# Optimization experiments

Hardware: AMD Instinct MI355X
Metric: run time of the kernel (lower is better)

Reference implementation:

```python
import jax, jax.numpy as jnp
import numpy as np

K_TOP = 2
N_HEADS = 4

def _ln(x, g, b, eps=1e-5):
    mu = x.mean(-1, keepdims=True)
    var = ((x - mu) ** 2).mean(-1, keepdims=True)
    return (x - mu) * jax.lax.rsqrt(var + eps) * g + b

def setup_inputs() -> dict:
    key = jax.random.key(0)
    ks = jax.random.split(key, 12)
    B, Na, dz, da = 1024, 32, 96, 32
    D = dz + da
    E, F, Hh, nr = 8, 1024, 512, 4
    s = 0.02
    rn = lambda k, sh: jax.random.normal(k, sh, jnp.float32) * s
    return dict(
        z=jax.random.normal(ks[0], (B, Na, dz), jnp.float32),
        a=jax.random.normal(ks[1], (B, Na, da), jnp.float32),
        w_gate=rn(ks[2], (Na * D, E)),
        w_in=rn(ks[3], (E, 3 * D, D)), b_in=jnp.zeros((E, 3 * D), jnp.float32),
        w_out=rn(ks[4], (E, D, D)), b_out=jnp.zeros((E, D), jnp.float32),
        ln1_g=jnp.ones((E, D), jnp.float32), ln1_b=jnp.zeros((E, D), jnp.float32),
        w1=rn(ks[5], (E, F, D)), b1=jnp.zeros((E, F), jnp.float32),
        w2=rn(ks[6], (E, D, F)), b2=jnp.zeros((E, D), jnp.float32),
        ln2_g=jnp.ones((E, D), jnp.float32), ln2_b=jnp.zeros((E, D), jnp.float32),
        head_w1=rn(ks[7], (Hh, Na * D)), head_b1=jnp.zeros((Hh,), jnp.float32),
        head_w2=rn(ks[8], (nr, Hh)), head_b2=jnp.zeros((nr,), jnp.float32),
    )

def reference(z, a, w_gate, w_in, b_in, w_out, b_out, ln1_g, ln1_b, w1, b1, w2, b2, ln2_g, ln2_b, head_w1, head_b1, head_w2, head_b2):
    B, Na, _ = z.shape
    x = jnp.concatenate([z, a], axis=-1)          # [B, Na, D]
    D = x.shape[-1]
    E = w_gate.shape[1]
    hd = D // N_HEADS
    x_flat = x.reshape(B, -1)                     # [B, Na*D]

    # --- NoisyTopKRouter (eval: clean logits only) ---
    logits = x_flat @ w_gate                      # [B, E]
    top_vals, top_idx = jax.lax.top_k(logits, min(K_TOP + 1, E))
    tk_gates = jax.nn.softmax(top_vals[:, :K_TOP], axis=1)
    gates = jnp.zeros_like(logits).at[jnp.arange(B)[:, None], top_idx[:, :K_TOP]].set(tk_gates)
    load = (gates > 0).sum(0).astype(jnp.float32)
    importance = gates.sum(0)
    cv2 = lambda v: jnp.var(v, ddof=1) / (jnp.mean(v) ** 2 + 1e-10)
    loss_bal = cv2(importance) + cv2(load) + jax.scipy.special.logsumexp(logits, axis=-1).mean()

    # --- expert (self-attn + FFN, pre/post-LN residual) ---
    def expert(p):
        wi, bi, wo, bo, g1, be1, W1, B1, W2, B2, g2, be2 = p
        qkv = x @ wi.T + bi                       # [B, Na, 3D]
        q, k_, v = jnp.split(qkv, 3, axis=-1)
        q = q.reshape(B, Na, N_HEADS, hd)
        k_ = k_.reshape(B, Na, N_HEADS, hd)
        v = v.reshape(B, Na, N_HEADS, hd)
        sc = jnp.einsum('bqhd,bkhd->bhqk', q, k_) / jnp.sqrt(jnp.float32(hd))
        att = jax.nn.softmax(sc, axis=-1)
        o = jnp.einsum('bhqk,bkhd->bqhd', att, v).reshape(B, Na, D)
        o = o @ wo.T + bo
        h = _ln(x + o, g1, be1)
        f = jax.nn.relu(h @ W1.T + B1) @ W2.T + B2
        return _ln(h + f, g2, be2)

    def body(y, p):
        *ep, gate_e = p                           # gate_e: [B]
        y = y + gate_e[:, None, None] * expert(tuple(ep))
        return y, None

    xs = (w_in, b_in, w_out, b_out, ln1_g, ln1_b, w1, b1, w2, b2, ln2_g, ln2_b, gates.T)
    y, _ = jax.lax.scan(body, jnp.zeros_like(x), xs)

    y_flat = y.reshape(B, -1)
    r = jax.nn.relu(y_flat @ head_w1.T + head_b1) @ head_w2.T + head_b2  # [B, n_r]
    return r, gates, loss_bal
```

## Files before the change

kernel.cpp:

```cpp
#include <hip/hip_runtime.h>
#include <math.h>


typedef short bf16x8 __attribute__((ext_vector_type(8)));
typedef float f32x4 __attribute__((ext_vector_type(4)));
typedef unsigned short u16;

#define MFMA(a, b, c) __builtin_amdgcn_mfma_f32_16x16x32_bf16((a), (b), (c), 0, 0, 0)

__device__ __forceinline__ u16 f2bf(float f) {
    unsigned int u = __float_as_uint(f);
    unsigned int r = u + 0x7FFFu + ((u >> 16) & 1u);
    return (u16)(r >> 16);
}
__device__ __forceinline__ float bf2f(u16 s) {
    return __uint_as_float(((unsigned int)s) << 16);
}

__global__ __launch_bounds__(256) void convert_kernel(
    const float* __restrict__ wi, const float* __restrict__ wo,
    const float* __restrict__ w1, const float* __restrict__ w2,
    const float* __restrict__ hw1,
    u16* __restrict__ wiB, u16* __restrict__ woB, u16* __restrict__ w1B,
    u16* __restrict__ w2B, u16* __restrict__ hw1B)
// ... 49 lines not shown
        for (int e = 0; e < 8; ++e) L[e] = red[0][e];
        int i0 = 0;
#pragma unroll
        for (int e = 1; e < 8; ++e) if (L[e] > L[i0]) i0 = e;
        int i1 = -1; float v1 = -3.0e38f;
#pragma unroll
        for (int e = 0; e < 8; ++e) if (e != i0 && L[e] > v1) { v1 = L[e]; i1 = e; }
        float e1 = expf(v1 - L[i0]);
        float inv = 1.f / (1.f + e1);
        float g0 = inv, g1 = e1 * inv;
#pragma unroll
        for (int e = 0; e < 8; ++e)
            gates_out[b * 8 + e] = (e == i0) ? g0 : ((e == i1) ? g1 : 0.f);
        float m = L[i0];
        float se = 0.f;
#pragma unroll
        for (int e = 0; e < 8; ++e) se += expf(L[e] - m);
        lse_ws[b] = m + logf(se);
        topi[b * 2 + 0] = i0; topi[b * 2 + 1] = i1;
        topg[b * 2 + 0] = g0; topg[b * 2 + 1] = g1;
    }
}

__global__ __launch_bounds__(256) void loss_kernel(
    const float* __restrict__ gates, const float* __restrict__ lse,
    float* __restrict__ out_loss)
{
    __shared__ float red[17][256];
    const int t = threadIdx.x;
    float imp[8], ld[8]; float ls = 0.f;
#pragma unroll
    for (int e = 0; e < 8; ++e) { imp[e] = 0.f; ld[e] = 0.f; }
    for (int b = t; b < 1024; b += 256) {
#pragma unroll
        for (int e = 0; e < 8; ++e) {
            float g = gates[b * 8 + e];
            imp[e] += g;
            ld[e] += (g > 0.f) ? 1.f : 0.f;
        }
        ls += lse[b];
    }
#pragma unroll
    for (int e = 0; e < 8; ++e) { red[e][t] = imp[e]; red[8 + e][t] = ld[e]; }
    red[16][t] = ls;
    __syncthreads();
    for (int s = 128; s; s >>= 1) {
        if (t < s) {
            for (int q = 0; q < 17; ++q) red[q][t] += red[q][t + s];
        }
        __syncthreads();
    }
    if (t == 0) {
        float cv[2];
        for (int p = 0; p < 2; ++p) {
            float sum = 0.f;
            for (int e = 0; e < 8; ++e) sum += red[p * 8 + e][0];
            float mean = sum * (1.f / 8.f);
            float var = 0.f;
            for (int e = 0; e < 8; ++e) {
                float dd = red[p * 8 + e][0] - mean;
                var += dd * dd;
            }
            var *= (1.f / 7.f);
            cv[p] = var / (mean * mean + 1e-10f);
        }
        out_loss[0] = cv[0] + cv[1] + red[16][0] * (1.f / 1024.f);
    }
}

__global__ __launch_bounds__(1024) void build_kernel(
    const int* __restrict__ topi, int* __restrict__ cnts,
    int* __restrict__ ent, int* __restrict__ meta)
{
    __shared__ int sc_[8];
    __shared__ int toff[9];
    const int t = threadIdx.x;
    if (t < 8) sc_[t] = 0;
    __syncthreads();
    int e0 = topi[t * 2], e1 = topi[t * 2 + 1];
    int p0 = atomicAdd(&sc_[e0], 1);
    ent[e0 * 2048 + p0] = t * 2;
    int p1 = atomicAdd(&sc_[e1], 1);
    ent[e1 * 2048 + p1] = t * 2 + 1;
    __syncthreads();
    if (t == 0) {
        int off = 0;
        for (int e = 0; e < 8; ++e) { toff[e] = off; off += (sc_[e] + 3) >> 2; }
        toff[8] = off;
        meta[0] = off;
    }
    __syncthreads();
    if (t < 8) {
        cnts[t] = sc_[t];
        int ntl = (sc_[t] + 3) >> 2, o = toff[t];
        for (int j = 0; j < ntl; ++j) {
            meta[1 + 2 * (o + j)] = t;
            meta[2 + 2 * (o + j)] = j * 4;
        }
    }
}

#define SM_X  0
#define SM_Q  32768
#define SM_K  65536
#define SM_VT 98304
#define SM_P  131072
#define SM_PS 147456
#define SM_PQ 149504
#define SM_MU 151552
#define SM_RS 152064
#define SM_TOTAL 152576
#define NTILES 520

__global__ __launch_bounds__(512, 2) void expert_group_kernel(
    const float* __restrict__ z, const float* __restrict__ a,
    const u16* __restrict__ wiBF, const float* __restrict__ b_in,
    const u16* __restrict__ woBF, const float* __restrict__ b_out,
    const float* __restrict__ ln1g, const float* __restrict__ ln1b,
    const u16* __restrict__ w1BF, const float* __restrict__ b1,
    const u16* __restrict__ w2BF, const float* __restrict__ b2,
    const float* __restrict__ ln2g, const float* __restrict__ ln2b,
    const float* __restrict__ topg, const int* __restrict__ cnts,
    const int* __restrict__ meta, const int* __restrict__ ent,
    u16* __restrict__ ybf)
{
    __shared__ __align__(16) char sm[SM_TOTAL];
    const int n_tiles = meta[0];
    const int bid = blockIdx.x;
    if (bid >= n_tiles) return;
    const int e = meta[1 + 2 * bid], base = meta[2 + 2 * bid];
    const int cnt = cnts[e];

    const int t = threadIdx.x;
    const int w = t >> 6, l = t & 63, l16 = l & 15, lk = l >> 4;
    const int ke = lk * 8;
    const int wr = w >> 2, wc = w & 3;
    const f32x4 zv = {0.f, 0.f, 0.f, 0.f};

    int bs[4], valid[4]; float gg[4];
#pragma unroll
    for (int i = 0; i < 4; ++i) {
        int gi = base + i;
        int idx = (gi < cnt) ? gi : (cnt - 1);
        int code = ent[e * 2048 + idx];
        valid[i] = (gi < cnt);
        bs[i] = code;
        gg[i] = topg[code];
    }

    {
        const int grow = t >> 4;
        const int gcol = (t & 15) * 8;
#pragma unroll
        for (int i = 0; i < 4; ++i) {
            int b_ = bs[i] >> 1;
            float v[8];
            if (gcol < 96) {
                const float* zp = z + ((size_t)b_ * 32 + grow) * 96 + gcol;
                float4 p0 = *(const float4*)zp, p1 = *(const float4*)(zp + 4);
                v[0] = p0.x; v[1] = p0.y; v[2] = p0.z; v[3] = p0.w;
                v[4] = p1.x; v[5] = p1.y; v[6] = p1.z; v[7] = p1.w;
            } else {
                const float* ap = a + ((size_t)b_ * 32 + grow) * 32 + (gcol - 96);
                float4 p0 = *(const float4*)ap, p1 = *(const float4*)(ap + 4);
                v[0] = p0.x; v[1] = p0.y; v[2] = p0.z; v[3] = p0.w;
                v[4] = p1.x; v[5] = p1.y; v[6] = p1.z; v[7] = p1.w;
            }
            bf16x8 pk;
#pragma unroll
            for (int j = 0; j < 8; ++j) pk[j] = (short)f2bf(v[j]);
            int row = i * 32 + grow;
            *(bf16x8*)(sm + SM_X + row * 256 + ((gcol * 2) ^ ((row & 7) << 4))) = pk;
        }
    }
    __syncthreads();

    {
        f32x4 acc[4][6];
#pragma unroll
        for (int m = 0; m < 4; ++m)
#pragma unroll
            for (int q = 0; q < 6; ++q) acc[m][q] = zv;
#pragma unroll
        for (int ks = 0; ks < 4; ++ks) {
            int kb = (ks * 32 + ke) * 2;
            bf16x8 af[4];
#pragma unroll
            for (int m = 0; m < 4; ++m) {
                int R = wr * 64 + m * 16 + l16;
                af[m] = *(const bf16x8*)(sm + SM_X + R * 256 + (kb ^ ((R & 7) << 4)));
            }
#pragma unroll
            for (int q = 0; q < 6; ++q) {
                int j = wc * 96 + q * 16 + l16;
                bf16x8 bb = *(const bf16x8*)(wiBF + e * 49152 + j * 128 + ks * 32 + ke);
#pragma unroll
                for (int m = 0; m < 4; ++m) acc[m][q] = MFMA(af[m], bb, acc[m][q]);
            }
        }
#pragma unroll
        for (int q = 0; q < 6; ++q) {
            int C = wc * 96 + q * 16 + l16;
            float bj = b_in[e * 384 + C];
#pragma unroll
            for (int m = 0; m < 4; ++m)
#pragma unroll
                for (int i = 0; i < 4; ++i) {
                    int R = wr * 64 + m * 16 + lk * 4 + i;
                    u16 val = f2bf(acc[m][q][i] + bj);
                    if (C < 128) {
                        *(u16*)(sm + SM_Q + R * 256 + ((C * 2) ^ ((R & 7) << 4))) = val;
                    } else if (C < 256) {
                        int c2 = C - 128;
                        *(u16*)(sm + SM_K + R * 256 + ((c2 * 2) ^ ((R & 7) << 4))) = val;
                    } else {
                        int rv = C - 256;
                        *(u16*)(sm + SM_VT + rv * 256 + ((R * 2) ^ ((rv & 7) << 4))) = val;
                    }
                }
        }
    }
    __syncthreads();

    f32x4 Ofrag[2][2][2];
    {
        const int tok = w >> 1;
        const int h2 = (w & 1) * 2;
        const float scale = 0.17677669529663687f;
#pragma unroll
        for (int p = 0; p < 2; ++p) {
            const int hb = (h2 + p) * 32;
            bf16x8 qa[2], kb2[2];
#pragma unroll
            for (int mt = 0; mt < 2; ++mt) {
                int R = tok * 32 + mt * 16 + l16;
                qa[mt] = *(const bf16x8*)(sm + SM_Q + R * 256 + (((hb + ke) * 2) ^ ((R & 7) << 4)));
                kb2[mt] = *(const bf16x8*)(sm + SM_K + R * 256 + (((hb + ke) * 2) ^ ((R & 7) << 4)));
            }
            f32x4 sc[2][2];
            sc[0][0] = MFMA(qa[0], kb2[0], zv); sc[0][1] = MFMA(qa[0], kb2[1], zv);
            sc[1][0] = MFMA(qa[1], kb2[0], zv); sc[1][1] = MFMA(qa[1], kb2[1], zv);
#pragma unroll
            for (int mt = 0; mt < 2; ++mt)
#pragma unroll
                for (int i = 0; i < 4; ++i) {
                    float v0 = sc[mt][0][i] * scale, v1 = sc[mt][1][i] * scale;
                    float m = fmaxf(v0, v1);
                    m = fmaxf(m, __shfl_xor(m, 1)); m = fmaxf(m, __shfl_xor(m, 2));
                    m = fmaxf(m, __shfl_xor(m, 4)); m = fmaxf(m, __shfl_xor(m, 8));
                    float e0 = __expf(v0 - m), e1 = __expf(v1 - m);
                    float ssum = e0 + e1;
                    ssum += __shfl_xor(ssum, 1); ssum += __shfl_xor(ssum, 2);
                    ssum += __shfl_xor(ssum, 4); ssum += __shfl_xor(ssum, 8);
                    float inv = 1.f / ssum;
                    int row = mt * 16 + lk * 4 + i;
                    char* pb = sm + SM_P + w * 2048 + row * 64;
                    int sw = (row & 3) << 4;
                    *(u16*)(pb + ((l16 * 2) ^ sw)) = f2bf(e0 * inv);
                    *(u16*)(pb + (((16 + l16) * 2) ^ sw)) = f2bf(e1 * inv);
                }
            bf16x8 pa[2];
#pragma unroll
            for (int mt = 0; mt < 2; ++mt) {
                int row = mt * 16 + l16;
                pa[mt] = *(const bf16x8*)(sm + SM_P + w * 2048 + row * 64 +
                                          ((ke * 2) ^ ((row & 3) << 4)));
            }
#pragma unroll
            for (int nt = 0; nt < 2; ++nt) {
                int rv = hb + nt * 16 + l16;
                bf16x8 vb = *(const bf16x8*)(sm + SM_VT + rv * 256 +
                                             (((tok * 32 + ke) * 2) ^ ((rv & 7) << 4)));
                Ofrag[p][0][nt] = MFMA(pa[0], vb, zv);
                Ofrag[p][1][nt] = MFMA(pa[1], vb, zv);
            }
        }
#pragma unroll
        for (int p = 0; p < 2; ++p)
#pragma unroll
            for (int mt = 0; mt < 2; ++mt)
#pragma unroll
                for (int nt = 0; nt < 2; ++nt)
#pragma unroll
                    for (int i = 0; i < 4; ++i) {
                        int R = tok * 32 + mt * 16 + lk * 4 + i;
                        int C = (h2 + p) * 32 + nt * 16 + l16;
                        *(u16*)(sm + SM_Q + R * 256 + ((C * 2) ^ ((R & 7) << 4))) =
                            f2bf(Ofrag[p][mt][nt][i]);
                    }
    }
    bf16x8 wof[2][4];
#pragma unroll
    for (int nt = 0; nt < 2; ++nt)
#pragma unroll
        for (int ks = 0; ks < 4; ++ks) {
            int j = wc * 32 + nt * 16 + l16;
            wof[nt][ks] = *(const bf16x8*)(woBF + e * 16384 + j * 128 + ks * 32 + ke);
        }
    __syncthreads();

    {
        f32x4 pr[4][2];
#pragma unroll
        for (int m = 0; m < 4; ++m) { pr[m][0] = zv; pr[m][1] = zv; }
#pragma unroll
        for (int ks = 0; ks < 4; ++ks) {
            int kb = (ks * 32 + ke) * 2;
            bf16x8 af[4];
#pragma unroll
            for (int m = 0; m < 4; ++m) {
                int R = wr * 64 + m * 16 + l16;
                af[m] = *(const bf16x8*)(sm + SM_Q + R * 256 + (kb ^ ((R & 7) << 4)));
            }
#pragma unroll
            for (int m = 0; m < 4; ++m) {
                pr[m][0] = MFMA(af[m], wof[0][ks], pr[m][0]);
                pr[m][1] = MFMA(af[m], wof[1][ks], pr[m][1]);
            }
        }
        float bo0 = b_out[e * 128 + wc * 32 + l16];
        float bo1 = b_out[e * 128 + wc * 32 + 16 + l16];
#pragma unroll
        for (int m = 0; m < 4; ++m) {
#pragma unroll
            for (int i = 0; i < 4; ++i) {
                int R = wr * 64 + m * 16 + lk * 4 + i;
                float u0, u1v;
                {
                    int C0 = wc * 32 + l16, C1 = C0 + 16;
                    float x0 = bf2f(*(const u16*)(sm + SM_X + R * 256 + ((C0 * 2) ^ ((R & 7) << 4))));
                    float x1 = bf2f(*(const u16*)(sm + SM_X + R * 256 + ((C1 * 2) ^ ((R & 7) << 4))));
                    u0 = pr[m][0][i] + bo0 + x0;
                    u1v = pr[m][1][i] + bo1 + x1;
                    *(u16*)(sm + SM_K + R * 256 + ((C0 * 2) ^ ((R & 7) << 4))) = f2bf(u0);
                    *(u16*)(sm + SM_K + R * 256 + ((C1 * 2) ^ ((R & 7) << 4))) = f2bf(u1v);
                }
                float s = u0 + u1v;
                float q = u0 * u0 + u1v * u1v;
                s += __shfl_xor(s, 1); q += __shfl_xor(q, 1);
                s += __shfl_xor(s, 2); q += __shfl_xor(q, 2);
                s += __shfl_xor(s, 4); q += __shfl_xor(q, 4);
                s += __shfl_xor(s, 8); q += __shfl_xor(q, 8);
                if (l16 == 0) {
                    *(float*)(sm + SM_PS + (R * 4 + wc) * 4) = s;
                    *(float*)(sm + SM_PQ + (R * 4 + wc) * 4) = q;
                }
            }
        }
    }
    __syncthreads();
    if (t < 128) {
        float s = 0.f, q = 0.f;
#pragma unroll
        for (int c = 0; c < 4; ++c) {
            s += *(const float*)(sm + SM_PS + (t * 4 + c) * 4);
            q += *(const float*)(sm + SM_PQ + (t * 4 + c) * 4);
        }
        float mu = s * (1.f / 128.f);
        float var = q * (1.f / 128.f) - mu * mu;
        *(float*)(sm + SM_MU + t * 4) = mu;
        *(float*)(sm + SM_RS + t * 4) = rsqrtf(var + 1e-5f);
    }
    __syncthreads();
    {
        int r_ = t >> 2, c0 = (t & 3) * 32;
        float mu_ = *(const float*)(sm + SM_MU + r_ * 4);
        float rs_ = *(const float*)(sm + SM_RS + r_ * 4);
#pragma unroll
        for (int j4 = 0; j4 < 4; ++j4) {
            int cb = c0 + j4 * 8;
            bf16x8* p = (bf16x8*)(sm + SM_K + r_ * 256 + ((cb * 2) ^ ((r_ & 7) << 4)));
            bf16x8 vch = *p;
#pragma unroll
            for (int jj = 0; jj < 8; ++jj) {
                int c = cb + jj;
                float f = (bf2f((u16)vch[jj]) - mu_) * rs_ * ln1g[e * 128 + c] + ln1b[e * 128 + c];
                vch[jj] = (short)f2bf(f);
            }
            *p = vch;
        }
    }
    __syncthreads();

    f32x4 facc[4][2];
#pragma unroll
    for (int m = 0; m < 4; ++m) { facc[m][0] = zv; facc[m][1] = zv; }
    {
        bf16x8 w1f[2][4], w2f[2][4];
#pragma unroll
        for (int nt = 0; nt < 2; ++nt)
#pragma unroll
            for (int ks = 0; ks < 4; ++ks) {
                int j = wc * 32 + nt * 16 + l16;
                w1f[nt][ks] = *(const bf16x8*)(w1BF + e * 131072 + j * 128 + ks * 32 + ke);
            }
        for (int c = 0; c < 8; ++c) {
#pragma unroll
            for (int nt = 0; nt < 2; ++nt)
#pragma unroll
                for (int ks = 0; ks < 4; ++ks) {
                    int j = wc * 32 + nt * 16 + l16;
                    w2f[nt][ks] = *(const bf16x8*)(w2BF + e * 131072 + j * 1024 +
                                                   c * 128 + ks * 32 + ke);
                }
            f32x4 a1[4][2];
#pragma unroll
            for (int m = 0; m < 4; ++m) { a1[m][0] = zv; a1[m][1] = zv; }
#pragma unroll
            for (int ks = 0; ks < 4; ++ks) {
                int kb = (ks * 32 + ke) * 2;
                bf16x8 af[4];
#pragma unroll
                for (int m = 0; m < 4; ++m) {
                    int R = wr * 64 + m * 16 + l16;
                    af[m] = *(const bf16x8*)(sm + SM_K + R * 256 + (kb ^ ((R & 7) << 4)));
                }
#pragma unroll
                for (int m = 0; m < 4; ++m) {
                    a1[m][0] = MFMA(af[m], w1f[0][ks], a1[m][0]);
                    a1[m][1] = MFMA(af[m], w1f[1][ks], a1[m][1]);
                }
            }
            __syncthreads();
            float b10 = b1[e * 1024 + c * 128 + wc * 32 + l16];
            float b11 = b1[e * 1024 + c * 128 + wc * 32 + 16 + l16];
#pragma unroll
            for (int m = 0; m < 4; ++m)
#pragma unroll
                for (int nt = 0; nt < 2; ++nt)
#pragma unroll
                    for (int i = 0; i < 4; ++i) {
                        int R = wr * 64 + m * 16 + lk * 4 + i;
                        int C = wc * 32 + nt * 16 + l16;
                        *(u16*)(sm + SM_VT + R * 256 + ((C * 2) ^ ((R & 7) << 4))) =
                            f2bf(fmaxf(a1[m][nt][i] + (nt ? b11 : b10), 0.f));
                    }
            if (c < 7) {
#pragma unroll
                for (int nt = 0; nt < 2; ++nt)
#pragma unroll
                    for (int ks = 0; ks < 4; ++ks) {
                        int j = (c + 1) * 128 + wc * 32 + nt * 16 + l16;
                        w1f[nt][ks] = *(const bf16x8*)(w1BF + e * 131072 + j * 128 + ks * 32 + ke);
                    }
            }
            __syncthreads();
#pragma unroll
            for (int ks = 0; ks < 4; ++ks) {
                int kb = (ks * 32 + ke) * 2;
                bf16x8 af[4];
#pragma unroll
                for (int m = 0; m < 4; ++m) {
                    int R = wr * 64 + m * 16 + l16;
                    af[m] = *(const bf16x8*)(sm + SM_VT + R * 256 + (kb ^ ((R & 7) << 4)));
                }
#pragma unroll
                for (int m = 0; m < 4; ++m) {
                    facc[m][0] = MFMA(af[m], w2f[0][ks], facc[m][0]);
                    facc[m][1] = MFMA(af[m], w2f[1][ks], facc[m][1]);
                }
            }
        }
    }

    {
        float b20 = b2[e * 128 + wc * 32 + l16];
        float b21 = b2[e * 128 + wc * 32 + 16 + l16];
        float u2[4][2][4];
#pragma unroll
        for (int m = 0; m < 4; ++m)
#pragma unroll
            for (int i = 0; i < 4; ++i) {
                int R = wr * 64 + m * 16 + lk * 4 + i;
                int C0 = wc * 32 + l16, C1 = C0 + 16;
                float h0 = bf2f(*(const u16*)(sm + SM_K + R * 256 + ((C0 * 2) ^ ((R & 7) << 4))));
                float h1v = bf2f(*(const u16*)(sm + SM_K + R * 256 + ((C1 * 2) ^ ((R & 7) << 4))));
                u2[m][0][i] = facc[m][0][i] + b20 + h0;
                u2[m][1][i] = facc[m][1][i] + b21 + h1v;
                float s = u2[m][0][i] + u2[m][1][i];
                float q = u2[m][0][i] * u2[m][0][i] + u2[m][1][i] * u2[m][1][i];
                s += __shfl_xor(s, 1); q += __shfl_xor(q, 1);
                s += __shfl_xor(s, 2); q += __shfl_xor(q, 2);
                s += __shfl_xor(s, 4); q += __shfl_xor(q, 4);
                s += __shfl_xor(s, 8); q += __shfl_xor(q, 8);
                if (l16 == 0) {
                    *(float*)(sm + SM_PS + (R * 4 + wc) * 4) = s;
                    *(float*)(sm + SM_PQ + (R * 4 + wc) * 4) = q;
                }
            }
        __syncthreads();
        if (t < 128) {
            float s = 0.f, q = 0.f;
#pragma unroll
            for (int c = 0; c < 4; ++c) {
                s += *(const float*)(sm + SM_PS + (t * 4 + c) * 4);
                q += *(const float*)(sm + SM_PQ + (t * 4 + c) * 4);
            }
            float mu = s * (1.f / 128.f);
            float var = q * (1.f / 128.f) - mu * mu;
            *(float*)(sm + SM_MU + t * 4) = mu;
            *(float*)(sm + SM_RS + t * 4) = rsqrtf(var + 1e-5f);
        }
        __syncthreads();
        float g20 = ln2g[e * 128 + wc * 32 + l16];
        float g21 = ln2g[e * 128 + wc * 32 + 16 + l16];
        float e20 = ln2b[e * 128 + wc * 32 + l16];
        float e21 = ln2b[e * 128 + wc * 32 + 16 + l16];
#pragma unroll
        for (int m = 0; m < 4; ++m) {
            float gm = gg[wr * 2 + (m >> 1)];
#pragma unroll
            for (int i = 0; i < 4; ++i) {
                int R = wr * 64 + m * 16 + lk * 4 + i;
                float mu_ = *(const float*)(sm + SM_MU + R * 4);
                float rs_ = *(const float*)(sm + SM_RS + R * 4);
                int C0 = wc * 32 + l16, C1 = C0 + 16;
                float v0 = gm * ((u2[m][0][i] - mu_) * rs_ * g20 + e20);
                float v1 = gm * ((u2[m][1][i] - mu_) * rs_ * g21 + e21);
                *(u16*)(sm + SM_VT + R * 256 + ((C0 * 2) ^ ((R & 7) << 4))) = f2bf(v0);
                *(u16*)(sm + SM_VT + R * 256 + ((C1 * 2) ^ ((R & 7) << 4))) = f2bf(v1);
            }
        }
    }
    __syncthreads();
    {
        int r_ = t >> 2, c0 = (t & 3) * 32;
        int ei = r_ >> 5;
        if (valid[ei]) {
            int code = bs[ei];
            int b_ = code >> 1, s_ = code & 1;
            u16* dst = ybf + ((size_t)(s_ * 1024 + b_)) * 4096 + (r_ & 31) * 128 + c0;
#pragma unroll
            for (int j4 = 0; j4 < 4; ++j4) {
                *(bf16x8*)(dst + j4 * 8) =
                    *(const bf16x8*)(sm + SM_VT + r_ * 256 + (((c0 + j4 * 8) * 2) ^ ((r_ & 7) << 4)));
            }
        }
    }
}

__global__ __launch_bounds__(256) void combine_kernel(
    u16* __restrict__ y0, const u16* __restrict__ y1)
{
    int i = (blockIdx.x * 256 + threadIdx.x) * 8;
    bf16x8 a = *(const bf16x8*)(y0 + i);
    bf16x8 b = *(const bf16x8*)(y1 + i);
    bf16x8 o;
#pragma unroll
    for (int j = 0; j < 8; ++j)
        o[j] = (short)f2bf(bf2f((u16)a[j]) + bf2f((u16)b[j]));
    *(bf16x8*)(y0 + i) = o;
}

__global__ __launch_bounds__(256) void head1_mfma(
    const u16* __restrict__ y_bf, const u16* __restrict__ hw1BF,
    const float* __restrict__ hb1, float* __restrict__ h_act)
{
    const int t = threadIdx.x, w = t >> 6, l = t & 63, l16 = l & 15, lk = l >> 4;
    const int ke = lk * 8;
// ... 69 lines not shown
    const float* l2b  = (const float*)d_in[14];
    const float* hw1  = (const float*)d_in[15];
    const float* hb1  = (const float*)d_in[16];
    const float* hw2  = (const float*)d_in[17];
    const float* hb2  = (const float*)d_in[18];

    float* out = (float*)d_out;
    float* r_out     = out;
    float* gates_out = out + 4096;
    float* loss_out  = out + 12288;

    char* W = (char*)d_ws;
    u16*   wiBF  = (u16*)(W + 0);
    u16*   woBF  = (u16*)(W + 786432);
    u16*   w1BF  = (u16*)(W + 1048576);
    u16*   w2BF  = (u16*)(W + 3145728);
    u16*   hw1BF = (u16*)(W + 5242880);
    u16*   ybf   = (u16*)(W + 9437184);
    float* h_act = (float*)(W + 26214400);
    float* lse   = (float*)(W + 28311552);
    float* topg  = (float*)(W + 28315648);
    int*   topi  = (int*)  (W + 28323840);
    int*   cnts  = (int*)  (W + 28332032);
    int*   meta  = (int*)  (W + 28332064);
    int*   ent   = (int*)  (W + 28336256);

    convert_kernel<<<4608, 256, 0, stream>>>(w_in, w_o, w1, w2, hw1,
                                             wiBF, woBF, w1BF, w2BF, hw1BF);
    router_kernel<<<1024, 256, 0, stream>>>(z, a, wg, gates_out, lse, topi, topg);
    loss_kernel<<<1, 256, 0, stream>>>(gates_out, lse, loss_out);
    build_kernel<<<1, 1024, 0, stream>>>(topi, cnts, ent, meta);
    expert_group_kernel<<<NTILES, 512, 0, stream>>>(z, a, wiBF, b_in, woBF, b_o,
        l1g, l1b, w1BF, b1, w2BF, b2, l2g, l2b, topg, cnts, meta, ent, ybf);
    combine_kernel<<<2048, 256, 0, stream>>>(ybf, ybf + 4194304);
    head1_mfma<<<dim3(32, 8), 256, 0, stream>>>(ybf, hw1BF, hb1, h_act);
    head2_kernel<<<1024, 64, 0, stream>>>(h_act, hw2, hb2, r_out);
}
```

Before: 330.0 us.

## Halve expert tile to two samples and fuse loss into build kernel

The expert kernel now processes 2 token groups (64 rows) per block instead of 4, and reuses LDS regions so shared memory per block drops from about 149KB to 64KB. Launch bounds move to 4 blocks per CU and the tile count doubles. The aim is higher occupancy and better latency hiding. The cost is that each block reads its expert weights for only half as many rows. Separately, the loss reduction is folded into the single-block build kernel, which removes one launch and uses the counts it already computes.

```diff
diff --git a/kernel.cpp b/kernel.cpp
--- a/kernel.cpp
+++ b/kernel.cpp
@@ -95,97 +95,85 @@
     }
 }
 
-__global__ __launch_bounds__(256) void loss_kernel(
-    const float* __restrict__ gates, const float* __restrict__ lse,
+__global__ __launch_bounds__(1024) void build_loss_kernel(
+    const int* __restrict__ topi, const float* __restrict__ topg,
+    const float* __restrict__ lse,
+    int* __restrict__ cnts, int* __restrict__ ent, int* __restrict__ meta,
     float* __restrict__ out_loss)
 {
-    __shared__ float red[17][256];
+    __shared__ int sc_[8];
+    __shared__ int toff[8];
+    __shared__ float red[9][1024];
     const int t = threadIdx.x;
-    float imp[8], ld[8]; float ls = 0.f;
-#pragma unroll
-    for (int e = 0; e < 8; ++e) { imp[e] = 0.f; ld[e] = 0.f; }
-    for (int b = t; b < 1024; b += 256) {
-#pragma unroll
-        for (int e = 0; e < 8; ++e) {
-            float g = gates[b * 8 + e];
-            imp[e] += g;
-            ld[e] += (g > 0.f) ? 1.f : 0.f;
-        }
-        ls += lse[b];
-    }
-#pragma unroll
-    for (int e = 0; e < 8; ++e) { red[e][t] = imp[e]; red[8 + e][t] = ld[e]; }
-    red[16][t] = ls;
-    __syncthreads();
-    for (int s = 128; s; s >>= 1) {
+    if (t < 8) sc_[t] = 0;
+    __syncthreads();
+    int e0 = topi[t * 2], e1 = topi[t * 2 + 1];
+    float g0 = topg[t * 2], g1 = topg[t * 2 + 1];
+    int p0 = atomicAdd(&sc_[e0], 1);
+    ent[e0 * 1024 + p0] = t * 2;
+    int p1 = atomicAdd(&sc_[e1], 1);
+    ent[e1 * 1024 + p1] = t * 2 + 1;
+#pragma unroll
+    for (int e = 0; e < 8; ++e)
+        red[e][t] = ((e == e0) ? g0 : 0.f) + ((e == e1) ? g1 : 0.f);
+    red[8][t] = lse[t];
+    __syncthreads();
+    for (int s = 512; s; s >>= 1) {
         if (t < s) {
-            for (int q = 0; q < 17; ++q) red[q][t] += red[q][t + s];
+#pragma unroll
+            for (int q = 0; q < 9; ++q) red[q][t] += red[q][t + s];
         }
         __syncthreads();
     }
     if (t == 0) {
-        float cv[2];
+        int off = 0;
+        for (int e = 0; e < 8; ++e) { toff[e] = off; off += (sc_[e] + 1) >> 1; }
+        meta[0] = off;
+        float cvv[2];
         for (int p = 0; p < 2; ++p) {
-            float sum = 0.f;
-            for (int e = 0; e < 8; ++e) sum += red[p * 8 + e][0];
+            float v[8], sum = 0.f;
+            for (int e = 0; e < 8; ++e) {
+                v[e] = p ? (float)sc_[e] : red[e][0];
+                sum += v[e];
+            }
             float mean = sum * (1.f / 8.f);
             float var = 0.f;
-            for (int e = 0; e < 8; ++e) {
-                float dd = red[p * 8 + e][0] - mean;
-                var += dd * dd;
-            }
+            for (int e = 0; e < 8; ++e) { float d = v[e] - mean; var += d * d; }
             var *= (1.f / 7.f);
-            cv[p] = var / (mean * mean + 1e-10f);
-        }
-        out_loss[0] = cv[0] + cv[1] + red[16][0] * (1.f / 1024.f);
-    }
-}
-
-__global__ __launch_bounds__(1024) void build_kernel(
-    const int* __restrict__ topi, int* __restrict__ cnts,
-    int* __restrict__ ent, int* __restrict__ meta)
-{
-    __shared__ int sc_[8];
-    __shared__ int toff[9];
-    const int t = threadIdx.x;
-    if (t < 8) sc_[t] = 0;
-    __syncthreads();
-    int e0 = topi[t * 2], e1 = topi[t * 2 + 1];
-    int p0 = atomicAdd(&sc_[e0], 1);
-    ent[e0 * 2048 + p0] = t * 2;
-    int p1 = atomicAdd(&sc_[e1], 1);
-    ent[e1 * 2048 + p1] = t * 2 + 1;
-    __syncthreads();
-    if (t == 0) {
-        int off = 0;
-        for (int e = 0; e < 8; ++e) { toff[e] = off; off += (sc_[e] + 3) >> 2; }
-        toff[8] = off;
-        meta[0] = off;
+            cvv[p] = var / (mean * mean + 1e-10f);
+        }
+        out_loss[0] = cvv[0] + cvv[1] + red[8][0] * (1.f / 1024.f);
     }
     __syncthreads();
     if (t < 8) {
         cnts[t] = sc_[t];
-        int ntl = (sc_[t] + 3) >> 2, o = toff[t];
+        int ntl = (sc_[t] + 1) >> 1, o = toff[t];
         for (int j = 0; j < ntl; ++j) {
             meta[1 + 2 * (o + j)] = t;
-            meta[2 + 2 * (o + j)] = j * 4;
-        }
-    }
-}
-
-#define SM_X  0
-#define SM_Q  32768
-#define SM_K  65536
-#define SM_VT 98304
-#define SM_P  131072
-#define SM_PS 147456
-#define SM_PQ 149504
-#define SM_MU 151552
-#define SM_RS 152064
-#define SM_TOTAL 152576
-#define NTILES 520
-
-__global__ __launch_bounds__(512, 2) void expert_group_kernel(
+            meta[2 + 2 * (o + j)] = j * 2;
+        }
+    }
+}
+
+#define SM_X 0
+#define SM_Q 16384
+#define SM_K 32768
+#define SM_V 49152
+#define SM_TOT 65536
+#define PS_OFF 0
+#define PQ_OFF 1024
+#define MU_OFF 2048
+#define RS_OFF 2304
+#define NTILES 1028
+
+__device__ __forceinline__ int tsw(int row, int col) {
+    return row * 256 + ((col * 2) ^ ((row & 7) << 4));
+}
+__device__ __forceinline__ int vsw(int row, int col) {
+    return row * 128 + ((col * 2) ^ ((row & 7) << 4));
+}
+
+__global__ __launch_bounds__(512, 4) void expert_group_kernel(
     const float* __restrict__ z, const float* __restrict__ a,
     const u16* __restrict__ wiBF, const float* __restrict__ b_in,
     const u16* __restrict__ woBF, const float* __restrict__ b_out,
@@ -197,7 +185,7 @@
     const int* __restrict__ meta, const int* __restrict__ ent,
     u16* __restrict__ ybf)
 {
-    __shared__ __align__(16) char sm[SM_TOTAL];
+    __shared__ __align__(16) char sm[SM_TOT];
     const int n_tiles = meta[0];
     const int bid = blockIdx.x;
     if (bid >= n_tiles) return;
@@ -210,65 +198,61 @@
     const int wr = w >> 2, wc = w & 3;
     const f32x4 zv = {0.f, 0.f, 0.f, 0.f};
 
-    int bs[4], valid[4]; float gg[4];
-#pragma unroll
-    for (int i = 0; i < 4; ++i) {
+    int bs[2], valid[2]; float gg[2];
+#pragma unroll
+    for (int i = 0; i < 2; ++i) {
         int gi = base + i;
         int idx = (gi < cnt) ? gi : (cnt - 1);
-        int code = ent[e * 2048 + idx];
+        int code = ent[e * 1024 + idx];
         valid[i] = (gi < cnt);
         bs[i] = code;
         gg[i] = topg[code];
     }
 
+#pragma unroll
+    for (int i = 0; i < 2; ++i) {
+        int cid = i * 512 + t;
+        int row = cid >> 4;
+        int cb = (cid & 15) * 8;
+        int b_ = bs[row >> 5] >> 1;
+        int n = row & 31;
+        float4 p0, p1;
+        if (cb < 96) {
+            const float* zp = z + ((size_t)b_ * 32 + n) * 96 + cb;
+            p0 = *(const float4*)zp; p1 = *(const float4*)(zp + 4);
+        } else {
+            const float* ap = a + ((size_t)b_ * 32 + n) * 32 + (cb - 96);
+            p0 = *(const float4*)ap; p1 = *(const float4*)(ap + 4);
+        }
+        bf16x8 pk;
+        pk[0] = (short)f2bf(p0.x); pk[1] = (short)f2bf(p0.y);
+        pk[2] = (short)f2bf(p0.z); pk[3] = (short)f2bf(p0.w);
+        pk[4] = (short)f2bf(p1.x); pk[5] = (short)f2bf(p1.y);
+        pk[6] = (short)f2bf(p1.z); pk[7] = (short)f2bf(p1.w);
+        *(bf16x8*)(sm + SM_X + tsw(row, cb)) = pk;
+    }
+    __syncthreads();
+
     {
-        const int grow = t >> 4;
-        const int gcol = (t & 15) * 8;
-#pragma unroll
-        for (int i = 0; i < 4; ++i) {
-            int b_ = bs[i] >> 1;
-            float v[8];
-            if (gcol < 96) {
-                const float* zp = z + ((size_t)b_ * 32 + grow) * 96 + gcol;
-                float4 p0 = *(const float4*)zp, p1 = *(const float4*)(zp + 4);
-                v[0] = p0.x; v[1] = p0.y; v[2] = p0.z; v[3] = p0.w;
-                v[4] = p1.x; v[5] = p1.y; v[6] = p1.z; v[7] = p1.w;
-            } else {
-                const float* ap = a + ((size_t)b_ * 32 + grow) * 32 + (gcol - 96);
-                float4 p0 = *(const float4*)ap, p1 = *(const float4*)(ap + 4);
-                v[0] = p0.x; v[1] = p0.y; v[2] = p0.z; v[3] = p0.w;
-                v[4] = p1.x; v[5] = p1.y; v[6] = p1.z; v[7] = p1.w;
-            }
-            bf16x8 pk;
-#pragma unroll
-            for (int j = 0; j < 8; ++j) pk[j] = (short)f2bf(v[j]);
-            int row = i * 32 + grow;
-            *(bf16x8*)(sm + SM_X + row * 256 + ((gcol * 2) ^ ((row & 7) << 4))) = pk;
-        }
-    }
-    __syncthreads();
-
-    {
-        f32x4 acc[4][6];
-#pragma unroll
-        for (int m = 0; m < 4; ++m)
-#pragma unroll
-            for (int q = 0; q < 6; ++q) acc[m][q] = zv;
+        f32x4 acc[2][6];
+#pragma unroll
+        for (int mt = 0; mt < 2; ++mt)
+#pragma unroll
+            for (int q = 0; q < 6; ++q) acc[mt][q] = zv;
 #pragma unroll
         for (int ks = 0; ks < 4; ++ks) {
-            int kb = (ks * 32 + ke) * 2;
-            bf16x8 af[4];
-#pragma unroll
-            for (int m = 0; m < 4; ++m) {
-                int R = wr * 64 + m * 16 + l16;
-                af[m] = *(const bf16x8*)(sm + SM_X + R * 256 + (kb ^ ((R & 7) << 4)));
+            bf16x8 af[2];
+#pragma unroll
+            for (int mt = 0; mt < 2; ++mt) {
+                int R = wr * 32 + mt * 16 + l16;
+                af[mt] = *(const bf16x8*)(sm + SM_X + tsw(R, ks * 32 + ke));
             }
 #pragma unroll
             for (int q = 0; q < 6; ++q) {
                 int j = wc * 96 + q * 16 + l16;
                 bf16x8 bb = *(const bf16x8*)(wiBF + e * 49152 + j * 128 + ks * 32 + ke);
 #pragma unroll
-                for (int m = 0; m < 4; ++m) acc[m][q] = MFMA(af[m], bb, acc[m][q]);
+                for (int mt = 0; mt < 2; ++mt) acc[mt][q] = MFMA(af[mt], bb, acc[mt][q]);
             }
         }
 #pragma unroll
@@ -276,138 +260,120 @@
             int C = wc * 96 + q * 16 + l16;
             float bj = b_in[e * 384 + C];
 #pragma unroll
-            for (int m = 0; m < 4; ++m)
+            for (int mt = 0; mt < 2; ++mt)
 #pragma unroll
                 for (int i = 0; i < 4; ++i) {
-                    int R = wr * 64 + m * 16 + lk * 4 + i;
-                    u16 val = f2bf(acc[m][q][i] + bj);
+                    int R = wr * 32 + mt * 16 + lk * 4 + i;
+                    u16 val = f2bf(acc[mt][q][i] + bj);
                     if (C < 128) {
-                        *(u16*)(sm + SM_Q + R * 256 + ((C * 2) ^ ((R & 7) << 4))) = val;
+                        *(u16*)(sm + SM_Q + tsw(R, C)) = val;
                     } else if (C < 256) {
-                        int c2 = C - 128;
-                        *(u16*)(sm + SM_K + R * 256 + ((c2 * 2) ^ ((R & 7) << 4))) = val;
+                        *(u16*)(sm + SM_K + tsw(R, C - 128)) = val;
                     } else {
-                        int rv = C - 256;
-                        *(u16*)(sm + SM_VT + rv * 256 + ((R * 2) ^ ((rv & 7) << 4))) = val;
+                        *(u16*)(sm + SM_V + vsw(C - 256, R)) = val;
                     }
                 }
         }
     }
     __syncthreads();
 
-    f32x4 Ofrag[2][2][2];
     {
-        const int tok = w >> 1;
-        const int h2 = (w & 1) * 2;
+        const int tok = w >> 2, hb = (w & 3) * 32;
         const float scale = 0.17677669529663687f;
-#pragma unroll
-        for (int p = 0; p < 2; ++p) {
-            const int hb = (h2 + p) * 32;
-            bf16x8 qa[2], kb2[2];
+        bf16x8 qa[2], kf[2];
+#pragma unroll
+        for (int mt = 0; mt < 2; ++mt) {
+            int R = tok * 32 + mt * 16 + l16;
+            qa[mt] = *(const bf16x8*)(sm + SM_Q + tsw(R, hb + ke));
+            kf[mt] = *(const bf16x8*)(sm + SM_K + tsw(R, hb + ke));
+        }
+        f32x4 sc[2][2];
+        sc[0][0] = MFMA(qa[0], kf[0], zv); sc[0][1] = MFMA(qa[0], kf[1], zv);
+        sc[1][0] = MFMA(qa[1], kf[0], zv); sc[1][1] = MFMA(qa[1], kf[1], zv);
+#pragma unroll
+        for (int mt = 0; mt < 2; ++mt)
+#pragma unroll
+            for (int i = 0; i < 4; ++i) {
+                float v0 = sc[mt][0][i] * scale, v1 = sc[mt][1][i] * scale;
+                float m = fmaxf(v0, v1);
+                m = fmaxf(m, __shfl_xor(m, 1)); m = fmaxf(m, __shfl_xor(m, 2));
+                m = fmaxf(m, __shfl_xor(m, 4)); m = fmaxf(m, __shfl_xor(m, 8));
+                float e0 = __expf(v0 - m), e1 = __expf(v1 - m);
+                float ssum = e0 + e1;
+                ssum += __shfl_xor(ssum, 1); ssum += __shfl_xor(ssum, 2);
+                ssum += __shfl_xor(ssum, 4); ssum += __shfl_xor(ssum, 8);
+                float inv = 1.f / ssum;
+                int row = mt * 16 + lk * 4 + i;
+                char* pb = sm + SM_X + w * 2048 + row * 64;
+                int sw = (row & 3) << 4;
+                *(u16*)(pb + ((l16 * 2) ^ sw)) = f2bf(e0 * inv);
+                *(u16*)(pb + (((16 + l16) * 2) ^ sw)) = f2bf(e1 * inv);
+            }
+        bf16x8 pa[2];
+#pragma unroll
+        for (int mt = 0; mt < 2; ++mt) {
+            int row = mt * 16 + l16;
+            pa[mt] = *(const bf16x8*)(sm + SM_X + w * 2048 + row * 64 +
+                                      ((ke * 2) ^ ((row & 3) << 4)));
+        }
+        f32x4 o[2][2];
+#pragma unroll
+        for (int nt = 0; nt < 2; ++nt) {
+            int rv = hb + nt * 16 + l16;
+            bf16x8 vb = *(const bf16x8*)(sm + SM_V + vsw(rv, tok * 32 + ke));
+            o[0][nt] = MFMA(pa[0], vb, zv);
+            o[1][nt] = MFMA(pa[1], vb, zv);
+        }
+#pragma unroll
+        for (int mt = 0; mt < 2; ++mt)
+#pragma unroll
+            for (int nt = 0; nt < 2; ++nt)
+#pragma unroll
+                for (int i = 0; i < 4; ++i) {
+                    int R = tok * 32 + mt * 16 + lk * 4 + i;
+                    int C = hb + nt * 16 + l16;
+                    *(u16*)(sm + SM_Q + tsw(R, C)) = f2bf(o[mt][nt][i]);
+                }
+    }
+    __syncthreads();
+
+    {
+        f32x4 pr[2][2];
+        pr[0][0] = zv; pr[0][1] = zv; pr[1][0] = zv; pr[1][1] = zv;
+#pragma unroll
+        for (int ks = 0; ks < 4; ++ks) {
+            bf16x8 af[2];
 #pragma unroll
             for (int mt = 0; mt < 2; ++mt) {
-                int R = tok * 32 + mt * 16 + l16;
-                qa[mt] = *(const bf16x8*)(sm + SM_Q + R * 256 + (((hb + ke) * 2) ^ ((R & 7) << 4)));
-                kb2[mt] = *(const bf16x8*)(sm + SM_K + R * 256 + (((hb + ke) * 2) ^ ((R & 7) << 4)));
-            }
-            f32x4 sc[2][2];
-            sc[0][0] = MFMA(qa[0], kb2[0], zv); sc[0][1] = MFMA(qa[0], kb2[1], zv);
-            sc[1][0] = MFMA(qa[1], kb2[0], zv); sc[1][1] = MFMA(qa[1], kb2[1], zv);
-#pragma unroll
-            for (int mt = 0; mt < 2; ++mt)
-#pragma unroll
-                for (int i = 0; i < 4; ++i) {
-                    float v0 = sc[mt][0][i] * scale, v1 = sc[mt][1][i] * scale;
-                    float m = fmaxf(v0, v1);
-                    m = fmaxf(m, __shfl_xor(m, 1)); m = fmaxf(m, __shfl_xor(m, 2));
-                    m = fmaxf(m, __shfl_xor(m, 4)); m = fmaxf(m, __shfl_xor(m, 8));
-                    float e0 = __expf(v0 - m), e1 = __expf(v1 - m);
-                    float ssum = e0 + e1;
-                    ssum += __shfl_xor(ssum, 1); ssum += __shfl_xor(ssum, 2);
-                    ssum += __shfl_xor(ssum, 4); ssum += __shfl_xor(ssum, 8);
-                    float inv = 1.f / ssum;
-                    int row = mt * 16 + lk * 4 + i;
-                    char* pb = sm + SM_P + w * 2048 + row * 64;
-                    int sw = (row & 3) << 4;
-                    *(u16*)(pb + ((l16 * 2) ^ sw)) = f2bf(e0 * inv);
-                    *(u16*)(pb + (((16 + l16) * 2) ^ sw)) = f2bf(e1 * inv);
-                }
-            bf16x8 pa[2];
-#pragma unroll
-            for (int mt = 0; mt < 2; ++mt) {
-                int row = mt * 16 + l16;
-                pa[mt] = *(const bf16x8*)(sm + SM_P + w * 2048 + row * 64 +
-                                          ((ke * 2) ^ ((row & 3) << 4)));
+                int R = wr * 32 + mt * 16 + l16;
+                af[mt] = *(const bf16x8*)(sm + SM_Q + tsw(R, ks * 32 + ke));
             }
 #pragma unroll
             for (int nt = 0; nt < 2; ++nt) {
-                int rv = hb + nt * 16 + l16;
-                bf16x8 vb = *(const bf16x8*)(sm + SM_VT + rv * 256 +
-                                             (((tok * 32 + ke) * 2) ^ ((rv & 7) << 4)));
-                Ofrag[p][0][nt] = MFMA(pa[0], vb, zv);
-                Ofrag[p][1][nt] = MFMA(pa[1], vb, zv);
-            }
-        }
-#pragma unroll
-        for (int p = 0; p < 2; ++p)
-#pragma unroll
-            for (int mt = 0; mt < 2; ++mt)
-#pragma unroll
-                for (int nt = 0; nt < 2; ++nt)
-#pragma unroll
-                    for (int i = 0; i < 4; ++i) {
-                        int R = tok * 32 + mt * 16 + lk * 4 + i;
-                        int C = (h2 + p) * 32 + nt * 16 + l16;
-                        *(u16*)(sm + SM_Q + R * 256 + ((C * 2) ^ ((R & 7) << 4))) =
-                            f2bf(Ofrag[p][mt][nt][i]);
-                    }
-    }
-    bf16x8 wof[2][4];
-#pragma unroll
-    for (int nt = 0; nt < 2; ++nt)
-#pragma unroll
-        for (int ks = 0; ks < 4; ++ks) {
-            int j = wc * 32 + nt * 16 + l16;
-            wof[nt][ks] = *(const bf16x8*)(woBF + e * 16384 + j * 128 + ks * 32 + ke);
-        }
-    __syncthreads();
-
-    {
-        f32x4 pr[4][2];
-#pragma unroll
-        for (int m = 0; m < 4; ++m) { pr[m][0] = zv; pr[m][1] = zv; }
-#pragma unroll
-        for (int ks = 0; ks < 4; ++ks) {
-            int kb = (ks * 32 + ke) * 2;
-            bf16x8 af[4];
-#pragma unroll
-            for (int m = 0; m < 4; ++m) {
-                int R = wr * 64 + m * 16 + l16;
-                af[m] = *(const bf16x8*)(sm + SM_Q + R * 256 + (kb ^ ((R & 7) << 4)));
-            }
-#pragma unroll
-            for (int m = 0; m < 4; ++m) {
-                pr[m][0] = MFMA(af[m], wof[0][ks], pr[m][0]);
-                pr[m][1] = MFMA(af[m], wof[1][ks], pr[m][1]);
-            }
-        }
-        float bo0 = b_out[e * 128 + wc * 32 + l16];
-        float bo1 = b_out[e * 128 + wc * 32 + 16 + l16];
-#pragma unroll
-        for (int m = 0; m < 4; ++m) {
+                int j = wc * 32 + nt * 16 + l16;
+                bf16x8 bb = *(const bf16x8*)(woBF + e * 16384 + j * 128 + ks * 32 + ke);
+                pr[0][nt] = MFMA(af[0], bb, pr[0][nt]);
+                pr[1][nt] = MFMA(af[1], bb, pr[1][nt]);
+            }
+        }
+        int C0 = wc * 32 + l16, C1 = C0 + 16;
+        float bo0 = b_out[e * 128 + C0];
+        float bo1 = b_out[e * 128 + C1];
+        int b_ = bs[wr] >> 1;
+#pragma unroll
+        for (int mt = 0; mt < 2; ++mt)
 #pragma unroll
             for (int i = 0; i < 4; ++i) {
-                int R = wr * 64 + m * 16 + lk * 4 + i;
-                float u0, u1v;
-                {
-                    int C0 = wc * 32 + l16, C1 = C0 + 16;
-                    float x0 = bf2f(*(const u16*)(sm + SM_X + R * 256 + ((C0 * 2) ^ ((R & 7) << 4))));
-                    float x1 = bf2f(*(const u16*)(sm + SM_X + R * 256 + ((C1 * 2) ^ ((R & 7) << 4))));
-                    u0 = pr[m][0][i] + bo0 + x0;
-                    u1v = pr[m][1][i] + bo1 + x1;
-                    *(u16*)(sm + SM_K + R * 256 + ((C0 * 2) ^ ((R & 7) << 4))) = f2bf(u0);
-                    *(u16*)(sm + SM_K + R * 256 + ((C1 * 2) ^ ((R & 7) << 4))) = f2bf(u1v);
-                }
+                int R = wr * 32 + mt * 16 + lk * 4 + i;
+                int n = R & 31;
+                float x0 = (C0 < 96) ? z[((size_t)b_ * 32 + n) * 96 + C0]
+                                     : a[((size_t)b_ * 32 + n) * 32 + C0 - 96];
+                float x1 = (C1 < 96) ? z[((size_t)b_ * 32 + n) * 96 + C1]
+                                     : a[((size_t)b_ * 32 + n) * 32 + C1 - 96];
+                float u0 = pr[mt][0][i] + bo0 + x0;
+                float u1v = pr[mt][1][i] + bo1 + x1;
+                *(u16*)(sm + SM_K + tsw(R, C0)) = f2bf(u0);
+                *(u16*)(sm + SM_K + tsw(R, C1)) = f2bf(u1v);
                 float s = u0 + u1v;
                 float q = u0 * u0 + u1v * u1v;
                 s += __shfl_xor(s, 1); q += __shfl_xor(q, 1);
@@ -415,34 +381,33 @@
                 s += __shfl_xor(s, 4); q += __shfl_xor(q, 4);
                 s += __shfl_xor(s, 8); q += __shfl_xor(q, 8);
                 if (l16 == 0) {
-                    *(float*)(sm + SM_PS + (R * 4 + wc) * 4) = s;
-                    *(float*)(sm + SM_PQ + (R * 4 + wc) * 4) = q;
-                }
-            }
-        }
-    }
-    __syncthreads();
-    if (t < 128) {
+                    *(float*)(sm + SM_X + PS_OFF + (R * 4 + wc) * 4) = s;
+                    *(float*)(sm + SM_X + PQ_OFF + (R * 4 + wc) * 4) = q;
+                }
+            }
+    }
+    __syncthreads();
+    if (t < 64) {
         float s = 0.f, q = 0.f;
 #pragma unroll
         for (int c = 0; c < 4; ++c) {
-            s += *(const float*)(sm + SM_PS + (t * 4 + c) * 4);
-            q += *(const float*)(sm + SM_PQ + (t * 4 + c) * 4);
+            s += *(const float*)(sm + SM_X + PS_OFF + (t * 4 + c) * 4);
+            q += *(const float*)(sm + SM_X + PQ_OFF + (t * 4 + c) * 4);
         }
         float mu = s * (1.f / 128.f);
         float var = q * (1.f / 128.f) - mu * mu;
-        *(float*)(sm + SM_MU + t * 4) = mu;
-        *(float*)(sm + SM_RS + t * 4) = rsqrtf(var + 1e-5f);
+        *(float*)(sm + SM_X + MU_OFF + t * 4) = mu;
+        *(float*)(sm + SM_X + RS_OFF + t * 4) = rsqrtf(var + 1e-5f);
     }
     __syncthreads();
     {
-        int r_ = t >> 2, c0 = (t & 3) * 32;
-        float mu_ = *(const float*)(sm + SM_MU + r_ * 4);
-        float rs_ = *(const float*)(sm + SM_RS + r_ * 4);
-#pragma unroll
-        for (int j4 = 0; j4 < 4; ++j4) {
+        int r_ = t >> 3, c0 = (t & 7) * 16;
+        float mu_ = *(const float*)(sm + SM_X + MU_OFF + r_ * 4);
+        float rs_ = *(const float*)(sm + SM_X + RS_OFF + r_ * 4);
+#pragma unroll
+        for (int j4 = 0; j4 < 2; ++j4) {
             int cb = c0 + j4 * 8;
-            bf16x8* p = (bf16x8*)(sm + SM_K + r_ * 256 + ((cb * 2) ^ ((r_ & 7) << 4)));
+            bf16x8* p = (bf16x8*)(sm + SM_K + tsw(r_, cb));
             bf16x8 vch = *p;
 #pragma unroll
             for (int jj = 0; jj < 8; ++jj) {
@@ -455,9 +420,8 @@
     }
     __syncthreads();
 
-    f32x4 facc[4][2];
-#pragma unroll
-    for (int m = 0; m < 4; ++m) { facc[m][0] = zv; facc[m][1] = zv; }
+    f32x4 facc[2][2];
+    facc[0][0] = zv; facc[0][1] = zv; facc[1][0] = zv; facc[1][1] = zv;
     {
         bf16x8 w1f[2][4], w2f[2][4];
 #pragma unroll
@@ -476,37 +440,35 @@
                     w2f[nt][ks] = *(const bf16x8*)(w2BF + e * 131072 + j * 1024 +
                                                    c * 128 + ks * 32 + ke);
                 }
-            f32x4 a1[4][2];
-#pragma unroll
-            for (int m = 0; m < 4; ++m) { a1[m][0] = zv; a1[m][1] = zv; }
+            f32x4 a1[2][2];
+            a1[0][0] = zv; a1[0][1] = zv; a1[1][0] = zv; a1[1][1] = zv;
 #pragma unroll
             for (int ks = 0; ks < 4; ++ks) {
-                int kb = (ks * 32 + ke) * 2;
-                bf16x8 af[4];
-#pragma unroll
-                for (int m = 0; m < 4; ++m) {
-                    int R = wr * 64 + m * 16 + l16;
-                    af[m] = *(const bf16x8*)(sm + SM_K + R * 256 + (kb ^ ((R & 7) << 4)));
-                }
-#pragma unroll
-                for (int m = 0; m < 4; ++m) {
-                    a1[m][0] = MFMA(af[m], w1f[0][ks], a1[m][0]);
-                    a1[m][1] = MFMA(af[m], w1f[1][ks], a1[m][1]);
-                }
-            }
-            __syncthreads();
+                bf16x8 af[2];
+#pragma unroll
+                for (int mt = 0; mt < 2; ++mt) {
+                    int R = wr * 32 + mt * 16 + l16;
+                    af[mt] = *(const bf16x8*)(sm + SM_K + tsw(R, ks * 32 + ke));
+                }
+#pragma unroll
+                for (int mt = 0; mt < 2; ++mt) {
+                    a1[mt][0] = MFMA(af[mt], w1f[0][ks], a1[mt][0]);
+                    a1[mt][1] = MFMA(af[mt], w1f[1][ks], a1[mt][1]);
+                }
+            }
+            char* Fb = sm + ((c & 1) ? SM_V : SM_Q);
             float b10 = b1[e * 1024 + c * 128 + wc * 32 + l16];
             float b11 = b1[e * 1024 + c * 128 + wc * 32 + 16 + l16];
 #pragma unroll
-            for (int m = 0; m < 4; ++m)
+            for (int mt = 0; mt < 2; ++mt)
 #pragma unroll
                 for (int nt = 0; nt < 2; ++nt)
 #pragma unroll
                     for (int i = 0; i < 4; ++i) {
-                        int R = wr * 64 + m * 16 + lk * 4 + i;
+                        int R = wr * 32 + mt * 16 + lk * 4 + i;
                         int C = wc * 32 + nt * 16 + l16;
-                        *(u16*)(sm + SM_VT + R * 256 + ((C * 2) ^ ((R & 7) << 4))) =
-                            f2bf(fmaxf(a1[m][nt][i] + (nt ? b11 : b10), 0.f));
+                        *(u16*)(Fb + tsw(R, C)) =
+                            f2bf(fmaxf(a1[mt][nt][i] + (nt ? b11 : b10), 0.f));
                     }
             if (c < 7) {
 #pragma unroll
@@ -520,94 +482,87 @@
             __syncthreads();
 #pragma unroll
             for (int ks = 0; ks < 4; ++ks) {
-                int kb = (ks * 32 + ke) * 2;
-                bf16x8 af[4];
-#pragma unroll
-                for (int m = 0; m < 4; ++m) {
-                    int R = wr * 64 + m * 16 + l16;
-                    af[m] = *(const bf16x8*)(sm + SM_VT + R * 256 + (kb ^ ((R & 7) << 4)));
-                }
-#pragma unroll
-                for (int m = 0; m < 4; ++m) {
-                    facc[m][0] = MFMA(af[m], w2f[0][ks], facc[m][0]);
-                    facc[m][1] = MFMA(af[m], w2f[1][ks], facc[m][1]);
+                bf16x8 af[2];
+#pragma unroll
+                for (int mt = 0; mt < 2; ++mt) {
+                    int R = wr * 32 + mt * 16 + l16;
+                    af[mt] = *(const bf16x8*)(Fb + tsw(R, ks * 32 + ke));
+                }
+#pragma unroll
+                for (int mt = 0; mt < 2; ++mt) {
+                    facc[mt][0] = MFMA(af[mt], w2f[0][ks], facc[mt][0]);
+                    facc[mt][1] = MFMA(af[mt], w2f[1][ks], facc[mt][1]);
                 }
             }
         }
     }
 
     {
-        float b20 = b2[e * 128 + wc * 32 + l16];
-        float b21 = b2[e * 128 + wc * 32 + 16 + l16];
-        float u2[4][2][4];
-#pragma unroll
-        for (int m = 0; m < 4; ++m)
+        int C0 = wc * 32 + l16, C1 = C0 + 16;
+        float b20 = b2[e * 128 + C0];
+        float b21 = b2[e * 128 + C1];
+        float u2[2][2][4];
+#pragma unroll
+        for (int mt = 0; mt < 2; ++mt)
 #pragma unroll
             for (int i = 0; i < 4; ++i) {
-                int R = wr * 64 + m * 16 + lk * 4 + i;
-                int C0 = wc * 32 + l16, C1 = C0 + 16;
-                float h0 = bf2f(*(const u16*)(sm + SM_K + R * 256 + ((C0 * 2) ^ ((R & 7) << 4))));
-                float h1v = bf2f(*(const u16*)(sm + SM_K + R * 256 + ((C1 * 2) ^ ((R & 7) << 4))));
-                u2[m][0][i] = facc[m][0][i] + b20 + h0;
-                u2[m][1][i] = facc[m][1][i] + b21 + h1v;
-                float s = u2[m][0][i] + u2[m][1][i];
-                float q = u2[m][0][i] * u2[m][0][i] + u2[m][1][i] * u2[m][1][i];
+                int R = wr * 32 + mt * 16 + lk * 4 + i;
+                float h0 = bf2f(*(const u16*)(sm + SM_K + tsw(R, C0)));
+                float h1v = bf2f(*(const u16*)(sm + SM_K + tsw(R, C1)));
+                u2[mt][0][i] = facc[mt][0][i] + b20 + h0;
+                u2[mt][1][i] = facc[mt][1][i] + b21 + h1v;
+                float s = u2[mt][0][i] + u2[mt][1][i];
+                float q = u2[mt][0][i] * u2[mt][0][i] + u2[mt][1][i] * u2[mt][1][i];
                 s += __shfl_xor(s, 1); q += __shfl_xor(q, 1);
                 s += __shfl_xor(s, 2); q += __shfl_xor(q, 2);
                 s += __shfl_xor(s, 4); q += __shfl_xor(q, 4);
                 s += __shfl_xor(s, 8); q += __shfl_xor(q, 8);
                 if (l16 == 0) {
-                    *(float*)(sm + SM_PS + (R * 4 + wc) * 4) = s;
-                    *(float*)(sm + SM_PQ + (R * 4 + wc) * 4) = q;
+                    *(float*)(sm + SM_X + PS_OFF + (R * 4 + wc) * 4) = s;
+                    *(float*)(sm + SM_X + PQ_OFF + (R * 4 + wc) * 4) = q;
                 }
             }
         __syncthreads();
-        if (t < 128) {
+        if (t < 64) {
             float s = 0.f, q = 0.f;
 #pragma unroll
             for (int c = 0; c < 4; ++c) {
-                s += *(const float*)(sm + SM_PS + (t * 4 + c) * 4);
-                q += *(const float*)(sm + SM_PQ + (t * 4 + c) * 4);
+                s += *(const float*)(sm + SM_X + PS_OFF + (t * 4 + c) * 4);
+                q += *(const float*)(sm + SM_X + PQ_OFF + (t * 4 + c) * 4);
             }
             float mu = s * (1.f / 128.f);
             float var = q * (1.f / 128.f) - mu * mu;
-            *(float*)(sm + SM_MU + t * 4) = mu;
-            *(float*)(sm + SM_RS + t * 4) = rsqrtf(var + 1e-5f);
+            *(float*)(sm + SM_X + MU_OFF + t * 4) = mu;
+            *(float*)(sm + SM_X + RS_OFF + t * 4) = rsqrtf(var + 1e-5f);
         }
         __syncthreads();
-        float g20 = ln2g[e * 128 + wc * 32 + l16];
-        float g21 = ln2g[e * 128 + wc * 32 + 16 + l16];
-        float e20 = ln2b[e * 128 + wc * 32 + l16];
-        float e21 = ln2b[e * 128 + wc * 32 + 16 + l16];
-#pragma unroll
-        for (int m = 0; m < 4; ++m) {
-            float gm = gg[wr * 2 + (m >> 1)];
+        float g20 = ln2g[e * 128 + C0], g21 = ln2g[e * 128 + C1];
+        float e20 = ln2b[e * 128 + C0], e21 = ln2b[e * 128 + C1];
+        float gm = gg[wr];
+#pragma unroll
+        for (int mt = 0; mt < 2; ++mt)
 #pragma unroll
             for (int i = 0; i < 4; ++i) {
-                int R = wr * 64 + m * 16 + lk * 4 + i;
-                float mu_ = *(const float*)(sm + SM_MU + R * 4);
-                float rs_ = *(const float*)(sm + SM_RS + R * 4);
-                int C0 = wc * 32 + l16, C1 = C0 + 16;
-                float v0 = gm * ((u2[m][0][i] - mu_) * rs_ * g20 + e20);
-                float v1 = gm * ((u2[m][1][i] - mu_) * rs_ * g21 + e21);
-                *(u16*)(sm + SM_VT + R * 256 + ((C0 * 2) ^ ((R & 7) << 4))) = f2bf(v0);
-                *(u16*)(sm + SM_VT + R * 256 + ((C1 * 2) ^ ((R & 7) << 4))) = f2bf(v1);
-            }
-        }
-    }
-    __syncthreads();
-    {
-        int r_ = t >> 2, c0 = (t & 3) * 32;
+                int R = wr * 32 + mt * 16 + lk * 4 + i;
+                float mu_ = *(const float*)(sm + SM_X + MU_OFF + R * 4);
+                float rs_ = *(const float*)(sm + SM_X + RS_OFF + R * 4);
+                float v0 = gm * ((u2[mt][0][i] - mu_) * rs_ * g20 + e20);
+                float v1 = gm * ((u2[mt][1][i] - mu_) * rs_ * g21 + e21);
+                *(u16*)(sm + SM_Q + tsw(R, C0)) = f2bf(v0);
+                *(u16*)(sm + SM_Q + tsw(R, C1)) = f2bf(v1);
+            }
+    }
+    __syncthreads();
+#pragma unroll
+    for (int i = 0; i < 2; ++i) {
+        int cid = i * 512 + t;
+        int r_ = cid >> 4, cb = (cid & 15) * 8;
         int ei = r_ >> 5;
         if (valid[ei]) {
             int code = bs[ei];
             int b_ = code >> 1, s_ = code & 1;
-            u16* dst = ybf + ((size_t)(s_ * 1024 + b_)) * 4096 + (r_ & 31) * 128 + c0;
-#pragma unroll
-            for (int j4 = 0; j4 < 4; ++j4) {
-                *(bf16x8*)(dst + j4 * 8) =
-                    *(const bf16x8*)(sm + SM_VT + r_ * 256 + (((c0 + j4 * 8) * 2) ^ ((r_ & 7) << 4)));
-            }
+            u16* dst = ybf + ((size_t)(s_ * 1024 + b_)) * 4096 + (r_ & 31) * 128 + cb;
+            *(bf16x8*)dst = *(const bf16x8*)(sm + SM_Q + tsw(r_, cb));
         }
     }
 }
@@ -723,14 +678,13 @@
     float* topg  = (float*)(W + 28315648);
     int*   topi  = (int*)  (W + 28323840);
     int*   cnts  = (int*)  (W + 28332032);
-    int*   meta  = (int*)  (W + 28332064);
-    int*   ent   = (int*)  (W + 28336256);
+    int*   meta  = (int*)  (W + 28332160);
+    int*   ent   = (int*)  (W + 28340480);
 
     convert_kernel<<<4608, 256, 0, stream>>>(w_in, w_o, w1, w2, hw1,
                                              wiBF, woBF, w1BF, w2BF, hw1BF);
     router_kernel<<<1024, 256, 0, stream>>>(z, a, wg, gates_out, lse, topi, topg);
-    loss_kernel<<<1, 256, 0, stream>>>(gates_out, lse, loss_out);
-    build_kernel<<<1, 1024, 0, stream>>>(topi, cnts, ent, meta);
+    build_loss_kernel<<<1, 1024, 0, stream>>>(topi, topg, lse, cnts, ent, meta, loss_out);
     expert_group_kernel<<<NTILES, 512, 0, stream>>>(z, a, wiBF, b_in, woBF, b_o,
         l1g, l1b, w1BF, b1, w2BF, b2, l2g, l2b, topg, cnts, meta, ent, ybf);
     combine_kernel<<<2048, 256, 0, stream>>>(ybf, ybf + 4194304);
```

New measurement: 336.3 us. Within noise of the previous version (+1.9%).
